# Kernel tuning notes

Measured on AMD Instinct MI355X. Metric: run time of the kernel, lower is better.

The kernel has to match this reference:

```python
import jax, jax.numpy as jnp
import numpy as np

B, T, IN, H, OUT = 256, 2048, 182, 64, 2


def setup_inputs() -> dict:
    key = jax.random.key(0)
    ks = jax.random.split(key, 7)
    x = jax.random.normal(ks[0], (B, T, IN), dtype=jnp.float32)
    # equinox GRUCell params: weight_ih (3H, IN), weight_hh (3H, H), bias (3H,), bias_n (H,)
    s_ih = 1.0 / np.sqrt(IN)
    s_hh = 1.0 / np.sqrt(H)
    weight_ih = jax.random.uniform(ks[1], (3 * H, IN), jnp.float32, -s_ih, s_ih)
    weight_hh = jax.random.uniform(ks[2], (3 * H, H), jnp.float32, -s_hh, s_hh)
    bias = jax.random.uniform(ks[3], (3 * H,), jnp.float32, -s_hh, s_hh)
    bias_n = jax.random.uniform(ks[4], (H,), jnp.float32, -s_hh, s_hh)
    # readout: Linear(H, OUT, use_bias=False) plus explicit zero-init bias param
    w_out = jax.random.uniform(ks[5], (OUT, H), jnp.float32, -s_hh, s_hh)
    out_bias = jnp.zeros((OUT,), dtype=jnp.float32)
    return {"x": x, "weight_ih": weight_ih, "weight_hh": weight_hh,
            "bias": bias, "bias_n": bias_n, "w_out": w_out, "out_bias": out_bias}


def reference(x, weight_ih, weight_hh, bias, bias_n, w_out, out_bias):
    # Batched GRU scan over time (vmap of the per-trial lax.scan in the module).
    def step(h, xt):  # h: (B,H), xt: (B,IN)
        ig = xt @ weight_ih.T + bias          # (B, 3H)
        hg = h @ weight_hh.T                  # (B, 3H)
        ir, iz, inew = jnp.split(ig, 3, axis=-1)
        hr, hz, hn = jnp.split(hg, 3, axis=-1)
        r = jax.nn.sigmoid(ir + hr)           # reset gate
        z = jax.nn.sigmoid(iz + hz)           # update gate (equinox 'inp')
        n = jnp.tanh(inew + r * (hn + bias_n))
        return n + z * (h - n), None

    h0 = jnp.zeros((x.shape[0], weight_hh.shape[1]), dtype=x.dtype)
    hT, _ = jax.lax.scan(step, h0, jnp.swapaxes(x, 0, 1))  # scan over T
    return jax.nn.sigmoid(hT @ w_out.T + out_bias)          # (B, OUT)
```

## Files before the change

kernel.cpp:

```cpp
#include <hip/hip_runtime.h>
#include <hip/hip_fp16.h>
#include <cstdint>
#include <cstddef>

#define BB  256
#define TT  2048
#define KIN 182
#define HH  64
#define G3  192
#define CH  16
#define NC  (TT/CH)

typedef _Float16 half8 __attribute__((ext_vector_type(8)));
typedef _Float16 h2v   __attribute__((ext_vector_type(2)));
typedef float    f32x4 __attribute__((ext_vector_type(4)));
typedef float    v2f   __attribute__((ext_vector_type(2)));

static __device__ __forceinline__ float dot2(h2v a, h2v b, float c) {
#if __has_builtin(__builtin_amdgcn_fdot2)
    return __builtin_amdgcn_fdot2(a, b, c, false);
#else
    return c + (float)a[0] * (float)b[0] + (float)a[1] * (float)b[1];
#endif
}

__global__ __launch_bounds__(128, 1) void gru_fused(
        const float* __restrict__ x,
        const float* __restrict__ wih,
        const float* __restrict__ whh,
        const float* __restrict__ bias,
        const float* __restrict__ bias_n,
        const float* __restrict__ wout,
        const float* __restrict__ outb,
        float* __restrict__ out)
{
    __shared__ float igb[2][CH][G3];
    __shared__ __align__(16) _Float16 hs[HH];

    const int tid  = threadIdx.x;
    const int lane = tid & 63;
    const int wid  = tid >> 6;
    const int b    = blockIdx.x;

    if (wid == 1) {
        const int col = lane & 15;
        const int kq  = lane >> 4;
        float bv[12];
#pragma unroll
        for (int nt = 0; nt < 12; ++nt) bv[nt] = bias[nt * 16 + col];

        const float* xb = x + (size_t)b * TT * KIN;

        auto produce = [&](int c, int buf) {
            const float* xr = xb + (size_t)(c * CH + col) * KIN;
            v2f xa[6][4];
#pragma unroll
            for (int kf = 0; kf < 6; ++kf)
#pragma unroll
                for (int j = 0; j < 4; ++j) {
                    int k = kf * 32 + kq * 8 + 2 * j;
                    v2f z2 = {0.f, 0.f};
                    xa[kf][j] = (k <= 180) ? *(const v2f*)(xr + k) : z2;
                }
            half8 af[6];
#pragma unroll
            for (int kf = 0; kf < 6; ++kf) {
                half8 t;
#pragma unroll
                for (int j = 0; j < 4; ++j) {
                    t[2 * j]     = (_Float16)xa[kf][j].x;
                    t[2 * j + 1] = (_Float16)xa[kf][j].y;
                }
                af[kf] = t;
            }
#pragma unroll
            for (int nt = 0; nt < 12; ++nt) {
                const float* wrow = wih + (size_t)(nt * 16 + col) * KIN + kq * 8;
                v2f bb[6][4];
#pragma unroll
                for (int kf = 0; kf < 6; ++kf)
#pragma unroll
                    for (int j = 0; j < 4; ++j) {
                        int k = kf * 32 + kq * 8 + 2 * j;
                        v2f z2 = {0.f, 0.f};
                        bb[kf][j] = (k <= 180) ? *(const v2f*)(wrow + kf * 32 + 2 * j) : z2;
                    }
                f32x4 cacc = {bv[nt], bv[nt], bv[nt], bv[nt]};
#pragma unroll
                for (int kf = 0; kf < 6; ++kf) {
                    half8 bt;
#pragma unroll
                    for (int j = 0; j < 4; ++j) {
                        bt[2 * j]     = (_Float16)bb[kf][j].x;
                        bt[2 * j + 1] = (_Float16)bb[kf][j].y;
                    }
                    cacc = __builtin_amdgcn_mfma_f32_16x16x32_f16(af[kf], bt, cacc, 0, 0, 0);
                }
                float* dst = &igb[buf][kq * 4][nt * 16 + col];
#pragma unroll
                for (int r = 0; r < 4; ++r) dst[r * G3] = cacc[r];
            }
        };

        produce(0, 0);
        __syncthreads();
        for (int c = 0; c < NC; ++c) {
            if (c + 1 < NC) produce(c + 1, (c + 1) & 1);
            __syncthreads();
        }
    } else {
        const int i = lane;
        h2v wr[32], wz[32], wn[32];
        {
            const v2f* pr = (const v2f*)(whh + (size_t)(0 * HH + i) * HH);
            const v2f* pz = (const v2f*)(whh + (size_t)(1 * HH + i) * HH);
            const v2f* pn = (const v2f*)(whh + (size_t)(2 * HH + i) * HH);
#pragma unroll
            for (int k = 0; k < 32; ++k) {
                v2f a = pr[k], c2 = pz[k], d2 = pn[k];
                h2v t;
                t[0] = (_Float16)a.x;  t[1] = (_Float16)a.y;  wr[k] = t;
                t[0] = (_Float16)c2.x; t[1] = (_Float16)c2.y; wz[k] = t;
                t[0] = (_Float16)d2.x; t[1] = (_Float16)d2.y; wn[k] = t;
            }
        }
        const float bn = bias_n[i];
        float h = 0.f;
        hs[i] = (_Float16)0.f;

        __syncthreads();

        for (int c = 0; c < NC; ++c) {
            const float* igrow = &igb[c & 1][0][0];
#pragma unroll 4
            for (int lt = 0; lt < CH; ++lt) {
                const float* p = igrow + lt * G3;
                float pr_ = p[i], pz_ = p[64 + i], pn_ = p[128 + i];
                float r0 = 0.f, r1 = 0.f, z0 = 0.f, z1 = 0.f, n0 = 0.f, n1 = 0.f;
                const half8* hp = (const half8*)hs;
#pragma unroll
                for (int q = 0; q < 8; ++q) {
                    half8 hv = hp[q];
                    h2v h0 = __builtin_shufflevector(hv, hv, 0, 1);
                    h2v h1 = __builtin_shufflevector(hv, hv, 2, 3);
                    h2v h2_ = __builtin_shufflevector(hv, hv, 4, 5);
                    h2v h3 = __builtin_shufflevector(hv, hv, 6, 7);
                    r0 = dot2(wr[4 * q + 0], h0, r0);
                    z0 = dot2(wz[4 * q + 0], h0, z0);
                    n0 = dot2(wn[4 * q + 0], h0, n0);
                    r1 = dot2(wr[4 * q + 1], h1, r1);
                    z1 = dot2(wz[4 * q + 1], h1, z1);
                    n1 = dot2(wn[4 * q + 1], h1, n1);
                    r0 = dot2(wr[4 * q + 2], h2_, r0);
                    z0 = dot2(wz[4 * q + 2], h2_, z0);
                    n0 = dot2(wn[4 * q + 2], h2_, n0);
                    r1 = dot2(wr[4 * q + 3], h3, r1);
                    z1 = dot2(wz[4 * q + 3], h3, z1);
                    n1 = dot2(wn[4 * q + 3], h3, n1);
                }
                float sr = r0 + r1, sz = z0 + z1, sn = n0 + n1;
                float r  = 1.f / (1.f + __expf(-(pr_ + sr)));
                float z  = 1.f / (1.f + __expf(-(pz_ + sz)));
                float e  = __expf(2.f * (pn_ + r * (sn + bn)));
                float nn = 1.f - 2.f / (e + 1.f);
                h = nn + z * (h - nn);
                __builtin_amdgcn_wave_barrier();
                hs[i] = (_Float16)h;
                __builtin_amdgcn_wave_barrier();
            }
            __syncthreads();
        }

        float s0 = wout[i] * h, s1 = wout[HH + i] * h;
#pragma unroll
        for (int off = 32; off > 0; off >>= 1) {
            s0 += __shfl_down(s0, off);
            s1 += __shfl_down(s1, off);
        }
        if (i == 0) {
            out[2 * b]     = 1.f / (1.f + __expf(-(s0 + outb[0])));
            out[2 * b + 1] = 1.f / (1.f + __expf(-(s1 + outb[1])));
        }
    }
}

extern "C" void kernel_launch(void* const* d_in, const int* in_sizes, int n_in,
                              void* d_out, int out_size, void* d_ws, size_t ws_size,
                              hipStream_t stream) {
    const float* x     = (const float*)d_in[0];
    const float* wih   = (const float*)d_in[1];
    const float* whh   = (const float*)d_in[2];
    const float* bias  = (const float*)d_in[3];
    const float* biasn = (const float*)d_in[4];
    const float* wout  = (const float*)d_in[5];
    const float* outb  = (const float*)d_in[6];
    float* out = (float*)d_out;
    (void)d_ws; (void)ws_size;

    gru_fused<<<BB, 128, 0, stream>>>(x, wih, whh, bias, biasn, wout, outb, out);
}
```

Before: 1.095 ms.

## Stage fp16 input weights in LDS and trim the recurrent step's serial latency

The producer wave now converts W_ih to fp16 once into padded shared memory. This replaces the global reload and reconversion of the weights for every chunk. The recurrent wave double-buffers the hidden state in LDS, which removes its wave barriers, and it prefetches the next timestep's input gates. It also uses inline v_dot2 asm and hardware reciprocal approximations for the sigmoid and tanh. The gate precomputations are padded to avoid bank conflicts. The cost is extra LDS use and slightly less accurate reciprocals.

```diff
diff --git a/kernel.cpp b/kernel.cpp
--- a/kernel.cpp
+++ b/kernel.cpp
@@ -10,18 +10,16 @@
 #define G3  192
 #define CH  16
 #define NC  (TT/CH)
+#define IGS 196
+#define BSS 200
 
 typedef _Float16 half8 __attribute__((ext_vector_type(8)));
 typedef _Float16 h2v   __attribute__((ext_vector_type(2)));
 typedef float    f32x4 __attribute__((ext_vector_type(4)));
 typedef float    v2f   __attribute__((ext_vector_type(2)));
 
-static __device__ __forceinline__ float dot2(h2v a, h2v b, float c) {
-#if __has_builtin(__builtin_amdgcn_fdot2)
-    return __builtin_amdgcn_fdot2(a, b, c, false);
-#else
-    return c + (float)a[0] * (float)b[0] + (float)a[1] * (float)b[1];
-#endif
+static __device__ __forceinline__ void dot2(float& acc, uint32_t a, uint32_t b) {
+    asm("v_dot2_f32_f16 %0, %1, %2, %0" : "+v"(acc) : "v"(a), "v"(b));
 }
 
 __global__ __launch_bounds__(128, 1) void gru_fused(
@@ -34,8 +32,9 @@
         const float* __restrict__ outb,
         float* __restrict__ out)
 {
-    __shared__ float igb[2][CH][G3];
-    __shared__ __align__(16) _Float16 hs[HH];
+    __shared__ float igb[2][CH][IGS];
+    __shared__ _Float16 Bs[G3][BSS];
+    __shared__ __align__(16) _Float16 hs[2][HH];
 
     const int tid  = threadIdx.x;
     const int lane = tid & 63;
@@ -45,6 +44,19 @@
     if (wid == 1) {
         const int col = lane & 15;
         const int kq  = lane >> 4;
+
+        for (int idx = lane; idx < G3 * 18; idx += 64) {
+            int n = idx / 18, k = KIN + (idx - n * 18);
+            Bs[n][k] = (_Float16)0.f;
+        }
+        for (int idx2 = lane; idx2 < G3 * KIN / 2; idx2 += 64) {
+            v2f a = ((const v2f*)wih)[idx2];
+            int e = 2 * idx2;
+            int n = e / KIN, k = e - n * KIN;
+            h2v t; t[0] = (_Float16)a.x; t[1] = (_Float16)a.y;
+            *(h2v*)&Bs[n][k] = t;
+        }
+
         float bv[12];
 #pragma unroll
         for (int nt = 0; nt < 12; ++nt) bv[nt] = bias[nt * 16 + col];
@@ -52,53 +64,49 @@
         const float* xb = x + (size_t)b * TT * KIN;
 
         auto produce = [&](int c, int buf) {
-            const float* xr = xb + (size_t)(c * CH + col) * KIN;
-            v2f xa[6][4];
-#pragma unroll
-            for (int kf = 0; kf < 6; ++kf)
+            const float* xr = xb + (size_t)(c * CH + col) * KIN + kq * 8;
+            half8 af[6];
+#pragma unroll
+            for (int kf = 0; kf < 5; ++kf) {
+                v2f a0 = *(const v2f*)(xr + kf * 32 + 0);
+                v2f a1 = *(const v2f*)(xr + kf * 32 + 2);
+                v2f a2 = *(const v2f*)(xr + kf * 32 + 4);
+                v2f a3 = *(const v2f*)(xr + kf * 32 + 6);
+                half8 t;
+                t[0] = (_Float16)a0.x; t[1] = (_Float16)a0.y;
+                t[2] = (_Float16)a1.x; t[3] = (_Float16)a1.y;
+                t[4] = (_Float16)a2.x; t[5] = (_Float16)a2.y;
+                t[6] = (_Float16)a3.x; t[7] = (_Float16)a3.y;
+                af[kf] = t;
+            }
+            {
+                v2f z2; z2.x = 0.f; z2.y = 0.f;
+                v2f a[4];
 #pragma unroll
                 for (int j = 0; j < 4; ++j) {
-                    int k = kf * 32 + kq * 8 + 2 * j;
-                    v2f z2 = {0.f, 0.f};
-                    xa[kf][j] = (k <= 180) ? *(const v2f*)(xr + k) : z2;
-                }
-            half8 af[6];
-#pragma unroll
-            for (int kf = 0; kf < 6; ++kf) {
+                    int k = 160 + kq * 8 + 2 * j;
+                    a[j] = (k <= 180) ? *(const v2f*)(xr + 160 + 2 * j) : z2;
+                }
                 half8 t;
 #pragma unroll
                 for (int j = 0; j < 4; ++j) {
-                    t[2 * j]     = (_Float16)xa[kf][j].x;
-                    t[2 * j + 1] = (_Float16)xa[kf][j].y;
-                }
-                af[kf] = t;
+                    t[2 * j]     = (_Float16)a[j].x;
+                    t[2 * j + 1] = (_Float16)a[j].y;
+                }
+                af[5] = t;
             }
 #pragma unroll
             for (int nt = 0; nt < 12; ++nt) {
-                const float* wrow = wih + (size_t)(nt * 16 + col) * KIN + kq * 8;
-                v2f bb[6][4];
-#pragma unroll
-                for (int kf = 0; kf < 6; ++kf)
-#pragma unroll
-                    for (int j = 0; j < 4; ++j) {
-                        int k = kf * 32 + kq * 8 + 2 * j;
-                        v2f z2 = {0.f, 0.f};
-                        bb[kf][j] = (k <= 180) ? *(const v2f*)(wrow + kf * 32 + 2 * j) : z2;
-                    }
-                f32x4 cacc = {bv[nt], bv[nt], bv[nt], bv[nt]};
+                const _Float16* br = &Bs[nt * 16 + col][kq * 8];
+                f32x4 c4 = {bv[nt], bv[nt], bv[nt], bv[nt]};
 #pragma unroll
                 for (int kf = 0; kf < 6; ++kf) {
-                    half8 bt;
-#pragma unroll
-                    for (int j = 0; j < 4; ++j) {
-                        bt[2 * j]     = (_Float16)bb[kf][j].x;
-                        bt[2 * j + 1] = (_Float16)bb[kf][j].y;
-                    }
-                    cacc = __builtin_amdgcn_mfma_f32_16x16x32_f16(af[kf], bt, cacc, 0, 0, 0);
+                    half8 bt = *(const half8*)(br + kf * 32);
+                    c4 = __builtin_amdgcn_mfma_f32_16x16x32_f16(af[kf], bt, c4, 0, 0, 0);
                 }
                 float* dst = &igb[buf][kq * 4][nt * 16 + col];
 #pragma unroll
-                for (int r = 0; r < 4; ++r) dst[r * G3] = cacc[r];
+                for (int r = 0; r < 4; ++r) dst[r * IGS] = c4[r];
             }
         };
 
@@ -110,7 +118,7 @@
         }
     } else {
         const int i = lane;
-        h2v wr[32], wz[32], wn[32];
+        uint32_t wr[32], wz[32], wn[32];
         {
             const v2f* pr = (const v2f*)(whh + (size_t)(0 * HH + i) * HH);
             const v2f* pz = (const v2f*)(whh + (size_t)(1 * HH + i) * HH);
@@ -119,54 +127,54 @@
             for (int k = 0; k < 32; ++k) {
                 v2f a = pr[k], c2 = pz[k], d2 = pn[k];
                 h2v t;
-                t[0] = (_Float16)a.x;  t[1] = (_Float16)a.y;  wr[k] = t;
-                t[0] = (_Float16)c2.x; t[1] = (_Float16)c2.y; wz[k] = t;
-                t[0] = (_Float16)d2.x; t[1] = (_Float16)d2.y; wn[k] = t;
+                t[0] = (_Float16)a.x;  t[1] = (_Float16)a.y;
+                wr[k] = __builtin_bit_cast(uint32_t, t);
+                t[0] = (_Float16)c2.x; t[1] = (_Float16)c2.y;
+                wz[k] = __builtin_bit_cast(uint32_t, t);
+                t[0] = (_Float16)d2.x; t[1] = (_Float16)d2.y;
+                wn[k] = __builtin_bit_cast(uint32_t, t);
             }
         }
         const float bn = bias_n[i];
         float h = 0.f;
-        hs[i] = (_Float16)0.f;
+        hs[0][i] = (_Float16)0.f;
 
         __syncthreads();
 
         for (int c = 0; c < NC; ++c) {
-            const float* igrow = &igb[c & 1][0][0];
+            const float* ig0 = &igb[c & 1][0][0];
+            float pr_ = ig0[i], pz_ = ig0[64 + i], pn_ = ig0[128 + i];
 #pragma unroll 4
             for (int lt = 0; lt < CH; ++lt) {
-                const float* p = igrow + lt * G3;
-                float pr_ = p[i], pz_ = p[64 + i], pn_ = p[128 + i];
+                const uint4* hp = (const uint4*)hs[lt & 1];
                 float r0 = 0.f, r1 = 0.f, z0 = 0.f, z1 = 0.f, n0 = 0.f, n1 = 0.f;
-                const half8* hp = (const half8*)hs;
 #pragma unroll
                 for (int q = 0; q < 8; ++q) {
-                    half8 hv = hp[q];
-                    h2v h0 = __builtin_shufflevector(hv, hv, 0, 1);
-                    h2v h1 = __builtin_shufflevector(hv, hv, 2, 3);
-                    h2v h2_ = __builtin_shufflevector(hv, hv, 4, 5);
-                    h2v h3 = __builtin_shufflevector(hv, hv, 6, 7);
-                    r0 = dot2(wr[4 * q + 0], h0, r0);
-                    z0 = dot2(wz[4 * q + 0], h0, z0);
-                    n0 = dot2(wn[4 * q + 0], h0, n0);
-                    r1 = dot2(wr[4 * q + 1], h1, r1);
-                    z1 = dot2(wz[4 * q + 1], h1, z1);
-                    n1 = dot2(wn[4 * q + 1], h1, n1);
-                    r0 = dot2(wr[4 * q + 2], h2_, r0);
-                    z0 = dot2(wz[4 * q + 2], h2_, z0);
-                    n0 = dot2(wn[4 * q + 2], h2_, n0);
-                    r1 = dot2(wr[4 * q + 3], h3, r1);
-                    z1 = dot2(wz[4 * q + 3], h3, z1);
-                    n1 = dot2(wn[4 * q + 3], h3, n1);
-                }
-                float sr = r0 + r1, sz = z0 + z1, sn = n0 + n1;
-                float r  = 1.f / (1.f + __expf(-(pr_ + sr)));
-                float z  = 1.f / (1.f + __expf(-(pz_ + sz)));
-                float e  = __expf(2.f * (pn_ + r * (sn + bn)));
-                float nn = 1.f - 2.f / (e + 1.f);
+                    uint4 hv = hp[q];
+                    dot2(r0, wr[4 * q + 0], hv.x);
+                    dot2(z0, wz[4 * q + 0], hv.x);
+                    dot2(n0, wn[4 * q + 0], hv.x);
+                    dot2(r1, wr[4 * q + 1], hv.y);
+                    dot2(z1, wz[4 * q + 1], hv.y);
+                    dot2(n1, wn[4 * q + 1], hv.y);
+                    dot2(r0, wr[4 * q + 2], hv.z);
+                    dot2(z0, wz[4 * q + 2], hv.z);
+                    dot2(n0, wn[4 * q + 2], hv.z);
+                    dot2(r1, wr[4 * q + 3], hv.w);
+                    dot2(z1, wz[4 * q + 3], hv.w);
+                    dot2(n1, wn[4 * q + 3], hv.w);
+                }
+                float cr = pr_, cz = pz_, cn = pn_;
+                if (lt != CH - 1) {
+                    const float* p = ig0 + (lt + 1) * IGS;
+                    pr_ = p[i]; pz_ = p[64 + i]; pn_ = p[128 + i];
+                }
+                float r  = __builtin_amdgcn_rcpf(1.f + __expf(-(cr + r0 + r1)));
+                float z  = __builtin_amdgcn_rcpf(1.f + __expf(-(cz + z0 + z1)));
+                float e  = __expf(2.f * (cn + r * ((n0 + n1) + bn)));
+                float nn = 1.f - 2.f * __builtin_amdgcn_rcpf(e + 1.f);
                 h = nn + z * (h - nn);
-                __builtin_amdgcn_wave_barrier();
-                hs[i] = (_Float16)h;
-                __builtin_amdgcn_wave_barrier();
+                hs[(lt & 1) ^ 1][i] = (_Float16)h;
             }
             __syncthreads();
         }
@@ -178,8 +186,8 @@
             s1 += __shfl_down(s1, off);
         }
         if (i == 0) {
-            out[2 * b]     = 1.f / (1.f + __expf(-(s0 + outb[0])));
-            out[2 * b + 1] = 1.f / (1.f + __expf(-(s1 + outb[1])));
+            out[2 * b]     = __builtin_amdgcn_rcpf(1.f + __expf(-(s0 + outb[0])));
+            out[2 * b + 1] = __builtin_amdgcn_rcpf(1.f + __expf(-(s1 + outb[1])));
         }
     }
 }
```

Result: slower. 1.204 ms (+9.9%).
